# Kernel optimization log

Hardware: AMD Instinct MI355X
Metric: run time of the kernel (lower is better)

The kernel has to match this reference:

```python
import jax, jax.numpy as jnp
import numpy as np

T, B, F, H, P = 256, 512, 256, 512, 12  # seq len, batch, feature_dim, hidden_dim, p_interval


def setup_inputs() -> dict:
    key = jax.random.key(0)
    ks = jax.random.split(key, 9)
    s = 1.0 / np.sqrt(F + H)  # torch Linear default init scale
    def lin(k):
        kw, kb = jax.random.split(k)
        W = jax.random.uniform(kw, (F + H, H), jnp.float32, -s, s)
        b = jax.random.uniform(kb, (H,), jnp.float32, -s, s)
        return W, b
    Wf, bf = lin(ks[0])
    Wi, bi = lin(ks[1])
    Wo, bo = lin(ks[2])
    Wg, bg = lin(ks[3])
    x = jax.random.normal(ks[4], (T, B, F), jnp.float32)
    return {"x": x, "Wf": Wf, "bf": bf, "Wi": Wi, "bi": bi,
            "Wo": Wo, "bo": bo, "Wg": Wg, "bg": bg}


def _slstm(x, Wf, bf, Wi, bi, Wo, bo, Wg, bg):
    Tn, Bn, _ = x.shape
    h0 = jnp.zeros((P, Bn, H), x.dtype)
    # NOTE: original torch code reassigns c to a 2D [B,H] tensor after step 0,
    # so c[t % P] indexes a batch ROW (shape [H]) that broadcasts. At t=0 the
    # slice is all-zeros either way, so carrying a 2D c is exactly faithful.
    c0 = jnp.zeros((Bn, H), x.dtype)

    def step(carry, inp):
        h, c = carry
        x_t, t = inp
        idx = t % P
        xc = jnp.concatenate([x_t, h[idx]], axis=1)  # [B, F+H]
        f = jax.nn.softmax(xc @ Wf + bf, axis=1)
        i = jax.nn.softmax(xc @ Wi + bi, axis=1)
        o = jax.nn.softmax(xc @ Wo + bo, axis=1)
        g = jnp.tanh(xc @ Wg + bg)
        c_new = jnp.tanh(f * c[idx] + i * g)  # c[idx]: row [H], broadcasts over B
        h = h.at[idx].set(o * c_new)
        return (h, c_new), None

    (h, _), _ = jax.lax.scan(step, (h0, c0), (x, jnp.arange(Tn)))
    return h[(Tn - 1) % P]


def reference(x, Wf, bf, Wi, bi, Wo, bo, Wg, bg):
    return _slstm(x, Wf, bf, Wi, bi, Wo, bo, Wg, bg)
```

## Files before the change

kernel.cpp:

```cpp
#include <hip/hip_runtime.h>

typedef unsigned short u16;
typedef unsigned int   u32;

typedef __attribute__((ext_vector_type(8))) short bf16x8;
typedef __attribute__((ext_vector_type(4))) float f32x4;

__device__ __forceinline__ u16 f2bf(float v) {
    u32 u = __float_as_uint(v);
    u32 r = (u + 0x7fffu + ((u >> 16) & 1u)) >> 16;
    return (u16)r;
}
__device__ __forceinline__ float bf2f(u16 h) { return __uint_as_float(((u32)h) << 16); }

__device__ __forceinline__ void gl2lds16(const void* g, void* l) {
    __builtin_amdgcn_global_load_lds(
        (const __attribute__((address_space(1))) void*)g,
        (__attribute__((address_space(3))) void*)l, 16, 0, 0);
}

__global__ void init_k(u16* __restrict__ hh, u16* __restrict__ hl, float* __restrict__ cb) {
    int i = blockIdx.x * 256 + threadIdx.x;
    hh[i] = 0; hl[i] = 0;
    if (i < 2 * 512) cb[i] = 0.0f;
}

__global__ void pack_w(const float* __restrict__ Wf, const float* __restrict__ bf_,
                       const float* __restrict__ Wi, const float* __restrict__ bi_,
                       const float* __restrict__ Wo, const float* __restrict__ bo_,
                       const float* __restrict__ Wg, const float* __restrict__ bg_,
                       u16* __restrict__ wth, u16* __restrict__ wtl, float* __restrict__ bias4) {
    int idx = blockIdx.x * 256 + threadIdx.x;
    int n = idx / 768, k = idx - n * 768;
    int gate = n >> 9, col = n & 511;
    const float* W = (gate == 0) ? Wf : (gate == 1) ? Wi : (gate == 2) ? Wo : Wg;
    float v = W[k * 512 + col];
    u16 h = f2bf(v);
    wth[idx] = h;
    wtl[idx] = f2bf(v - bf2f(h));
    if (k == 0) {
        const float* bb = (gate == 0) ? bf_ : (gate == 1) ? bi_ : (gate == 2) ? bo_ : bg_;
        bias4[n] = bb[col];
    }
}

__global__ void split_x(const float* __restrict__ src, u16* __restrict__ oh, u16* __restrict__ ol) {
    int i = blockIdx.x * 256 + threadIdx.x;
    float4 v = ((const float4*)src)[i];
    u16 hx = f2bf(v.x), hy = f2bf(v.y), hz = f2bf(v.z), hw = f2bf(v.w);
    u16 lx = f2bf(v.x - bf2f(hx)), ly = f2bf(v.y - bf2f(hy));
    u16 lz = f2bf(v.z - bf2f(hz)), lw = f2bf(v.w - bf2f(hw));
    uint2 hv; hv.x = (u32)hx | ((u32)hy << 16); hv.y = (u32)hz | ((u32)hw << 16);
    uint2 lv; lv.x = (u32)lx | ((u32)ly << 16); lv.y = (u32)lz | ((u32)lw << 16);
    ((uint2*)oh)[i] = hv;
    ((uint2*)ol)[i] = lv;
}

#define BK 32
__global__ __launch_bounds__(256, 3) void gemm_x3(
    const u16* __restrict__ xh, const u16* __restrict__ xl,
    const u16* __restrict__ hh, const u16* __restrict__ hl,
    const u16* __restrict__ wth, const u16* __restrict__ wtl,
    const float* __restrict__ bias4, float* __restrict__ lg) {
    __shared__ __align__(16) u16 Ah[128 * BK];
    __shared__ __align__(16) u16 Al[128 * BK];
    __shared__ __align__(16) u16 Bh[128 * BK];
    __shared__ __align__(16) u16 Bl[128 * BK];

    const int tid = threadIdx.x;
    const int wid = tid >> 6, lane = tid & 63;
    const int bn = blockIdx.x, bm = blockIdx.y;
    const int s = bm >> 2;
    const int b0 = (bm & 3) * 128;
    const int laneR = lane >> 2;
    const int laneC = (lane & 3) * 8;

    u16* lds = (wid == 0) ? Ah : (wid == 1) ? Al : (wid == 2) ? Bh : Bl;
    const u16* xp = (wid == 0) ? xh : xl;
    const u16* hp = (wid == 0) ? hh : hl;
    const u16* wp = (wid == 2) ? wth : wtl;
    const u16* xrow = xp + (size_t)(s * 512 + b0) * 256 + laneR * 256 + laneC;
    const u16* hrow = hp + (size_t)(s * 512 + b0) * 512 + laneR * 512 + laneC;
    const u16* wrow = wp + (size_t)(bn * 128) * 768 + laneR * 768 + laneC;

    const int wm = wid >> 1, wn = wid & 1;
    const int lm = lane & 15, quad = lane >> 4;

    f32x4 acc[4][4];
#pragma unroll
    for (int i = 0; i < 4; i++)
#pragma unroll
        for (int j = 0; j < 4; j++) { acc[i][j].x = 0.f; acc[i][j].y = 0.f; acc[i][j].z = 0.f; acc[i][j].w = 0.f; }

    for (int k0 = 0; k0 < 768; k0 += BK) {
        __syncthreads();
        if (wid < 2) {
            if (k0 < 256) {
                const u16* src = xrow + k0;
#pragma unroll
                for (int r = 0; r < 8; ++r) gl2lds16(src + r * 16 * 256, lds + r * 16 * BK);
            } else {
                const u16* src = hrow + (k0 - 256);
#pragma unroll
                for (int r = 0; r < 8; ++r) gl2lds16(src + r * 16 * 512, lds + r * 16 * BK);
            }
        } else {
            const u16* src = wrow + k0;
#pragma unroll
            for (int r = 0; r < 8; ++r) gl2lds16(src + r * 16 * 768, lds + r * 16 * BK);
        }
        __syncthreads();

        bf16x8 a_h[4], a_l[4], b_h[4], b_l[4];
#pragma unroll
        for (int i = 0; i < 4; ++i) {
            a_h[i] = *(const bf16x8*)&Ah[(wm * 64 + i * 16 + lm) * BK + quad * 8];
            a_l[i] = *(const bf16x8*)&Al[(wm * 64 + i * 16 + lm) * BK + quad * 8];
            b_h[i] = *(const bf16x8*)&Bh[(wn * 64 + i * 16 + lm) * BK + quad * 8];
            b_l[i] = *(const bf16x8*)&Bl[(wn * 64 + i * 16 + lm) * BK + quad * 8];
        }
#pragma unroll
        for (int i = 0; i < 4; ++i)
#pragma unroll
            for (int j = 0; j < 4; ++j) {
                acc[i][j] = __builtin_amdgcn_mfma_f32_16x16x32_bf16(a_h[i], b_h[j], acc[i][j], 0, 0, 0);
                acc[i][j] = __builtin_amdgcn_mfma_f32_16x16x32_bf16(a_h[i], b_l[j], acc[i][j], 0, 0, 0);
                acc[i][j] = __builtin_amdgcn_mfma_f32_16x16x32_bf16(a_l[i], b_h[j], acc[i][j], 0, 0, 0);
            }
    }

#pragma unroll
    for (int j = 0; j < 4; ++j) {
        int n = bn * 128 + wn * 64 + j * 16 + lm;
        float bv = bias4[n];
#pragma unroll
        for (int i = 0; i < 4; ++i) {
            int row = wm * 64 + i * 16 + quad * 4;
            size_t base = (size_t)(bm * 128 + row) * 2048 + n;
#pragma unroll
            for (int r = 0; r < 4; ++r) lg[base + (size_t)r * 2048] = acc[i][j][r] + bv;
        }
    }
}

__device__ __forceinline__ void chain_step(const float* __restrict__ lg, int j, int lane, float r[8]) {
    int rowb = (j + 1) % 12;
    const float* base = lg + (size_t)(j * 512 + rowb) * 2048 + lane * 8;
    float f[8], iv[8], g[8];
#pragma unroll
    for (int u = 0; u < 8; ++u) { f[u] = base[u]; iv[u] = base[512 + u]; g[u] = base[1536 + u]; }
    float mf = -1e30f, mi = -1e30f;
#pragma unroll
    for (int u = 0; u < 8; ++u) { mf = fmaxf(mf, f[u]); mi = fmaxf(mi, iv[u]); }
#pragma unroll
    for (int o = 32; o; o >>= 1) { mf = fmaxf(mf, __shfl_xor(mf, o)); mi = fmaxf(mi, __shfl_xor(mi, o)); }
    float sf = 0.f, si = 0.f;
#pragma unroll
    for (int u = 0; u < 8; ++u) {
        f[u] = __expf(f[u] - mf); sf += f[u];
        iv[u] = __expf(iv[u] - mi); si += iv[u];
    }
#pragma unroll
    for (int o = 32; o; o >>= 1) { sf += __shfl_xor(sf, o); si += __shfl_xor(si, o); }
    float rf = 1.0f / sf, ri = 1.0f / si;
#pragma unroll
    for (int u = 0; u < 8; ++u) {
        float gg = tanhf(g[u]);
        r[u] = tanhf(f[u] * rf * r[u] + iv[u] * ri * gg);
    }
}

__global__ __launch_bounds__(256) void gates_k(
    const float* __restrict__ lg, float* __restrict__ cb,
    u16* __restrict__ hh, u16* __restrict__ hl,
    float* __restrict__ out, int t0, int S, int rd, int wr) {
    __shared__ float rsh[512];
    const int widx = threadIdx.x >> 6, lane = threadIdx.x & 63;
    const int s = blockIdx.x >> 7;
    const int b = (blockIdx.x & 127) * 4 + widx;
    const int t = t0 + s;

    if (widx == 0) {
        float r[8];
#pragma unroll
        for (int u = 0; u < 8; ++u) r[u] = cb[rd * 512 + lane * 8 + u];
        for (int j = 0; j < s; ++j) chain_step(lg, j, lane, r);
#pragma unroll
        for (int u = 0; u < 8; ++u) rsh[lane * 8 + u] = r[u];
        if ((int)blockIdx.x == S * 128 - 1 && t0 + S < 256) {
            chain_step(lg, s, lane, r);
#pragma unroll
            for (int u = 0; u < 8; ++u) cb[wr * 512 + lane * 8 + u] = r[u];
        }
    }
    __syncthreads();

    const float* row = lg + (size_t)(s * 512 + b) * 2048 + lane * 8;
    float f[8], iv[8], ov[8], g[8];
#pragma unroll
    for (int u = 0; u < 8; ++u) {
        f[u] = row[u]; iv[u] = row[512 + u]; ov[u] = row[1024 + u]; g[u] = row[1536 + u];
    }
    float mf = -1e30f, mi = -1e30f, mo = -1e30f;
#pragma unroll
    for (int u = 0; u < 8; ++u) { mf = fmaxf(mf, f[u]); mi = fmaxf(mi, iv[u]); mo = fmaxf(mo, ov[u]); }
#pragma unroll
    for (int o = 32; o; o >>= 1) {
        mf = fmaxf(mf, __shfl_xor(mf, o));
        mi = fmaxf(mi, __shfl_xor(mi, o));
        mo = fmaxf(mo, __shfl_xor(mo, o));
    }
    float sf = 0.f, si = 0.f, so = 0.f;
#pragma unroll
    for (int u = 0; u < 8; ++u) {
        f[u] = __expf(f[u] - mf); sf += f[u];
        iv[u] = __expf(iv[u] - mi); si += iv[u];
        ov[u] = __expf(ov[u] - mo); so += ov[u];
    }
#pragma unroll
    for (int o = 32; o; o >>= 1) {
        sf += __shfl_xor(sf, o); si += __shfl_xor(si, o); so += __shfl_xor(so, o);
    }
    float rf = 1.0f / sf, ri = 1.0f / si, ro = 1.0f / so;
    float hout[8];
#pragma unroll
    for (int u = 0; u < 8; ++u) {
        float rr = rsh[lane * 8 + u];
        float gg = tanhf(g[u]);
        float cv = tanhf(f[u] * rf * rr + iv[u] * ri * gg);
        hout[u] = ov[u] * ro * cv;
    }
    u32 hhp[4], hlp[4];
#pragma unroll
    for (int u = 0; u < 4; ++u) {
        u16 h0 = f2bf(hout[2 * u]), h1 = f2bf(hout[2 * u + 1]);
        u16 l0 = f2bf(hout[2 * u] - bf2f(h0)), l1 = f2bf(hout[2 * u + 1] - bf2f(h1));
        hhp[u] = (u32)h0 | ((u32)h1 << 16);
        hlp[u] = (u32)l0 | ((u32)l1 << 16);
    }
    size_t hb = ((size_t)(s * 512 + b)) * 512 + lane * 8;
    *(uint4*)&hh[hb] = make_uint4(hhp[0], hhp[1], hhp[2], hhp[3]);
    *(uint4*)&hl[hb] = make_uint4(hlp[0], hlp[1], hlp[2], hlp[3]);
    if (t == 255) {
        float* op = out + (size_t)b * 512 + lane * 8;
#pragma unroll
        for (int u = 0; u < 8; ++u) op[u] = hout[u];
    }
}

extern "C" void kernel_launch(void* const* d_in, const int* in_sizes, int n_in,
                              void* d_out, int out_size, void* d_ws, size_t ws_size,
                              hipStream_t stream) {
    const float* x   = (const float*)d_in[0];
    const float* Wf  = (const float*)d_in[1];
    const float* bf_ = (const float*)d_in[2];
    const float* Wi  = (const float*)d_in[3];
    const float* bi_ = (const float*)d_in[4];
    const float* Wo  = (const float*)d_in[5];
    const float* bo_ = (const float*)d_in[6];
    const float* Wg  = (const float*)d_in[7];
    const float* bg_ = (const float*)d_in[8];
    float* out = (float*)d_out;

    char* p = (char*)d_ws;
    u16* xh  = (u16*)p; p += 134217728;
    u16* xl  = (u16*)p; p += 134217728;
    u16* wth = (u16*)p; p += 3145728;
    u16* wtl = (u16*)p; p += 3145728;
    u16* hh  = (u16*)p; p += 6291456;
    u16* hl  = (u16*)p; p += 6291456;
    float* bias4 = (float*)p; p += 8192;
    float* cb    = (float*)p; p += 4096;
    float* lg    = (float*)p; p += 50331648;

    init_k<<<12288, 256, 0, stream>>>(hh, hl, cb);
    pack_w<<<6144, 256, 0, stream>>>(Wf, bf_, Wi, bi_, Wo, bo_, Wg, bg_, wth, wtl, bias4);
    split_x<<<32768, 256, 0, stream>>>(x, xh, xl);

    for (int blk = 0; blk < 22; ++blk) {
        int t0 = blk * 12;
        int S = (256 - t0 >= 12) ? 12 : (256 - t0);
        gemm_x3<<<dim3(16, S * 4), 256, 0, stream>>>(
            xh + (size_t)t0 * 512 * 256, xl + (size_t)t0 * 512 * 256,
            hh, hl, wth, wtl, bias4, lg);
        gates_k<<<S * 128, 256, 0, stream>>>(lg, cb, hh, hl, out, t0, S, blk & 1, (blk + 1) & 1);
    }
}
```

Measured before the change: 2.154 ms.

## Switch GEMM to 32x32 MFMA, fast tanh/rcp, reorder grid and gate blocks

The split-bf16 GEMM moves from 16x16x32 to 32x32x16 MFMA tiles, which changes the register fragment layout and the epilogue mapping. Epilogue stores become nontemporal, and the grid axes are swapped so M tiles vary fastest. In the gates kernel, tanhf and division are replaced by an exp/rcp based tanh and hardware reciprocals. Gate blocks are launched in reverse timestep order so the blocks with the longest serial chain start first. The approximate tanh and rcp may reduce accuracy slightly.

```diff
diff --git a/kernel.cpp b/kernel.cpp
--- a/kernel.cpp
+++ b/kernel.cpp
@@ -4,7 +4,7 @@
 typedef unsigned int   u32;
 
 typedef __attribute__((ext_vector_type(8))) short bf16x8;
-typedef __attribute__((ext_vector_type(4))) float f32x4;
+typedef __attribute__((ext_vector_type(16))) float f32x16;
 
 __device__ __forceinline__ u16 f2bf(float v) {
     u32 u = __float_as_uint(v);
@@ -12,6 +12,11 @@
     return (u16)r;
 }
 __device__ __forceinline__ float bf2f(u16 h) { return __uint_as_float(((u32)h) << 16); }
+
+__device__ __forceinline__ float ftanh(float x) {
+    float e = __expf(2.0f * x);
+    return 1.0f - 2.0f * __builtin_amdgcn_rcpf(e + 1.0f);
+}
 
 __device__ __forceinline__ void gl2lds16(const void* g, void* l) {
     __builtin_amdgcn_global_load_lds(
@@ -69,7 +74,7 @@
 
     const int tid = threadIdx.x;
     const int wid = tid >> 6, lane = tid & 63;
-    const int bn = blockIdx.x, bm = blockIdx.y;
+    const int bm = blockIdx.x, bn = blockIdx.y;
     const int s = bm >> 2;
     const int b0 = (bm & 3) * 128;
     const int laneR = lane >> 2;
@@ -84,13 +89,15 @@
     const u16* wrow = wp + (size_t)(bn * 128) * 768 + laneR * 768 + laneC;
 
     const int wm = wid >> 1, wn = wid & 1;
-    const int lm = lane & 15, quad = lane >> 4;
-
-    f32x4 acc[4][4];
-#pragma unroll
-    for (int i = 0; i < 4; i++)
-#pragma unroll
-        for (int j = 0; j < 4; j++) { acc[i][j].x = 0.f; acc[i][j].y = 0.f; acc[i][j].z = 0.f; acc[i][j].w = 0.f; }
+    const int l32 = lane & 31, khalf = lane >> 5;
+
+    f32x16 acc[2][2];
+#pragma unroll
+    for (int i = 0; i < 2; i++)
+#pragma unroll
+        for (int j = 0; j < 2; j++)
+#pragma unroll
+            for (int r = 0; r < 16; ++r) acc[i][j][r] = 0.f;
 
     for (int k0 = 0; k0 < 768; k0 += BK) {
         __syncthreads();
@@ -111,34 +118,42 @@
         }
         __syncthreads();
 
-        bf16x8 a_h[4], a_l[4], b_h[4], b_l[4];
-#pragma unroll
-        for (int i = 0; i < 4; ++i) {
-            a_h[i] = *(const bf16x8*)&Ah[(wm * 64 + i * 16 + lm) * BK + quad * 8];
-            a_l[i] = *(const bf16x8*)&Al[(wm * 64 + i * 16 + lm) * BK + quad * 8];
-            b_h[i] = *(const bf16x8*)&Bh[(wn * 64 + i * 16 + lm) * BK + quad * 8];
-            b_l[i] = *(const bf16x8*)&Bl[(wn * 64 + i * 16 + lm) * BK + quad * 8];
-        }
-#pragma unroll
-        for (int i = 0; i < 4; ++i)
-#pragma unroll
-            for (int j = 0; j < 4; ++j) {
-                acc[i][j] = __builtin_amdgcn_mfma_f32_16x16x32_bf16(a_h[i], b_h[j], acc[i][j], 0, 0, 0);
-                acc[i][j] = __builtin_amdgcn_mfma_f32_16x16x32_bf16(a_h[i], b_l[j], acc[i][j], 0, 0, 0);
-                acc[i][j] = __builtin_amdgcn_mfma_f32_16x16x32_bf16(a_l[i], b_h[j], acc[i][j], 0, 0, 0);
+        bf16x8 a_h[2][2], a_l[2][2], b_h[2][2], b_l[2][2];
+#pragma unroll
+        for (int t = 0; t < 2; ++t)
+#pragma unroll
+            for (int ks = 0; ks < 2; ++ks) {
+                int ko = ks * 16 + khalf * 8;
+                a_h[t][ks] = *(const bf16x8*)&Ah[(wm * 64 + t * 32 + l32) * BK + ko];
+                a_l[t][ks] = *(const bf16x8*)&Al[(wm * 64 + t * 32 + l32) * BK + ko];
+                b_h[t][ks] = *(const bf16x8*)&Bh[(wn * 64 + t * 32 + l32) * BK + ko];
+                b_l[t][ks] = *(const bf16x8*)&Bl[(wn * 64 + t * 32 + l32) * BK + ko];
             }
-    }
-
-#pragma unroll
-    for (int j = 0; j < 4; ++j) {
-        int n = bn * 128 + wn * 64 + j * 16 + lm;
+#pragma unroll
+        for (int ks = 0; ks < 2; ++ks)
+#pragma unroll
+            for (int i = 0; i < 2; ++i)
+#pragma unroll
+                for (int j = 0; j < 2; ++j) {
+                    acc[i][j] = __builtin_amdgcn_mfma_f32_32x32x16_bf16(a_h[i][ks], b_h[j][ks], acc[i][j], 0, 0, 0);
+                    acc[i][j] = __builtin_amdgcn_mfma_f32_32x32x16_bf16(a_h[i][ks], b_l[j][ks], acc[i][j], 0, 0, 0);
+                    acc[i][j] = __builtin_amdgcn_mfma_f32_32x32x16_bf16(a_l[i][ks], b_h[j][ks], acc[i][j], 0, 0, 0);
+                }
+    }
+
+#pragma unroll
+    for (int j = 0; j < 2; ++j) {
+        int n = bn * 128 + wn * 64 + j * 32 + l32;
         float bv = bias4[n];
 #pragma unroll
-        for (int i = 0; i < 4; ++i) {
-            int row = wm * 64 + i * 16 + quad * 4;
-            size_t base = (size_t)(bm * 128 + row) * 2048 + n;
-#pragma unroll
-            for (int r = 0; r < 4; ++r) lg[base + (size_t)r * 2048] = acc[i][j][r] + bv;
+        for (int i = 0; i < 2; ++i) {
+            int rbase = wm * 64 + i * 32 + 4 * khalf;
+#pragma unroll
+            for (int r = 0; r < 16; ++r) {
+                int row = rbase + (r & 3) + 8 * (r >> 2);
+                __builtin_nontemporal_store(acc[i][j][r] + bv,
+                    &lg[(size_t)(bm * 128 + row) * 2048 + n]);
+            }
         }
     }
 }
@@ -162,11 +177,11 @@
     }
 #pragma unroll
     for (int o = 32; o; o >>= 1) { sf += __shfl_xor(sf, o); si += __shfl_xor(si, o); }
-    float rf = 1.0f / sf, ri = 1.0f / si;
-#pragma unroll
-    for (int u = 0; u < 8; ++u) {
-        float gg = tanhf(g[u]);
-        r[u] = tanhf(f[u] * rf * r[u] + iv[u] * ri * gg);
+    float rf = __builtin_amdgcn_rcpf(sf), ri = __builtin_amdgcn_rcpf(si);
+#pragma unroll
+    for (int u = 0; u < 8; ++u) {
+        float gg = ftanh(g[u]);
+        r[u] = ftanh(f[u] * rf * r[u] + iv[u] * ri * gg);
     }
 }
 
@@ -176,7 +191,7 @@
     float* __restrict__ out, int t0, int S, int rd, int wr) {
     __shared__ float rsh[512];
     const int widx = threadIdx.x >> 6, lane = threadIdx.x & 63;
-    const int s = blockIdx.x >> 7;
+    const int s = (S - 1) - (blockIdx.x >> 7);
     const int b = (blockIdx.x & 127) * 4 + widx;
     const int t = t0 + s;
 
@@ -187,8 +202,8 @@
         for (int j = 0; j < s; ++j) chain_step(lg, j, lane, r);
 #pragma unroll
         for (int u = 0; u < 8; ++u) rsh[lane * 8 + u] = r[u];
-        if ((int)blockIdx.x == S * 128 - 1 && t0 + S < 256) {
-            chain_step(lg, s, lane, r);
+        if ((int)blockIdx.x == 127 && t0 + S < 256) {
+            chain_step(lg, S - 1, lane, r);
 #pragma unroll
             for (int u = 0; u < 8; ++u) cb[wr * 512 + lane * 8 + u] = r[u];
         }
@@ -221,13 +236,13 @@
     for (int o = 32; o; o >>= 1) {
         sf += __shfl_xor(sf, o); si += __shfl_xor(si, o); so += __shfl_xor(so, o);
     }
-    float rf = 1.0f / sf, ri = 1.0f / si, ro = 1.0f / so;
+    float rf = __builtin_amdgcn_rcpf(sf), ri = __builtin_amdgcn_rcpf(si), ro = __builtin_amdgcn_rcpf(so);
     float hout[8];
 #pragma unroll
     for (int u = 0; u < 8; ++u) {
         float rr = rsh[lane * 8 + u];
-        float gg = tanhf(g[u]);
-        float cv = tanhf(f[u] * rf * rr + iv[u] * ri * gg);
+        float gg = ftanh(g[u]);
+        float cv = ftanh(f[u] * rf * rr + iv[u] * ri * gg);
         hout[u] = ov[u] * ro * cv;
     }
     u32 hhp[4], hlp[4];
@@ -280,7 +295,7 @@
     for (int blk = 0; blk < 22; ++blk) {
         int t0 = blk * 12;
         int S = (256 - t0 >= 12) ? 12 : (256 - t0);
-        gemm_x3<<<dim3(16, S * 4), 256, 0, stream>>>(
+        gemm_x3<<<dim3(S * 4, 16), 256, 0, stream>>>(
             xh + (size_t)t0 * 512 * 256, xl + (size_t)t0 * 512 * 256,
             hh, hl, wth, wtl, bias4, lg);
         gates_k<<<S * 128, 256, 0, stream>>>(lg, cb, hh, hl, out, t0, S, blk & 1, (blk + 1) & 1);
```

After: 1.975 ms. 8.3% less time.
